# Optimization experiments

Measured on AMD Instinct MI355X. Metric: run time of the kernel, lower is better.

The kernel has to match this reference:

```python
import jax, jax.numpy as jnp
import numpy as np

N_HEAD = 8
N_FEAT = 512
D_HEAD = N_FEAT // N_HEAD


def setup_inputs() -> dict:
    key = jax.random.key(0)
    ks = jax.random.split(key, 11)
    B, T, L = 4, 2048, 16
    s = 1.0 / np.sqrt(D_HEAD)
    so = 1.0 / np.sqrt(N_FEAT)
    return {
        "q": jax.random.normal(ks[0], (B, T, 1, N_FEAT), jnp.float32),
        "k": jax.random.normal(ks[1], (B, T, L, N_FEAT), jnp.float32),
        "v": jax.random.normal(ks[2], (B, T, L, N_FEAT), jnp.float32),
        "Wq": jax.random.uniform(ks[3], (D_HEAD, D_HEAD), jnp.float32, -s, s),
        "bq": jax.random.uniform(ks[4], (D_HEAD,), jnp.float32, -s, s),
        "Wk": jax.random.uniform(ks[5], (D_HEAD, D_HEAD), jnp.float32, -s, s),
        "bk": jax.random.uniform(ks[6], (D_HEAD,), jnp.float32, -s, s),
        "Wv": jax.random.uniform(ks[7], (D_HEAD, D_HEAD), jnp.float32, -s, s),
        "bv": jax.random.uniform(ks[8], (D_HEAD,), jnp.float32, -s, s),
        "Wo": jax.random.uniform(ks[9], (N_FEAT, N_FEAT), jnp.float32, -so, so),
        "bo": jax.random.uniform(ks[10], (N_FEAT,), jnp.float32, -so, so),
    }


def reference(q, k, v, Wq, bq, Wk, bk, Wv, bv, Wo, bo):
    B, T, L, F = k.shape
    H, D = N_HEAD, D_HEAD
    # split heads: q [B,T,H,D] (query axis of length 1 squeezed), k/v [B,T,L,H,D]
    qh = q.reshape(B, T, H, D)
    kh = k.reshape(B, T, L, H, D)
    vh = v.reshape(B, T, L, H, D)
    # per-head linear projections (shared across heads), Linear: x @ W^T + b
    qh = jnp.einsum("bthd,ed->bthe", qh, Wq) + bq
    kh = jnp.einsum("btlhd,ed->btlhe", kh, Wk) + bk
    vh = jnp.einsum("btlhd,ed->btlhe", vh, Wv) + bv
    # attention scores over the local window L (query length 1 per timestep)
    attw = jnp.einsum("bthd,btlhd->bthl", qh, kh) / jnp.sqrt(jnp.asarray(D, qh.dtype))
    attn = jax.nn.softmax(attw, axis=-1)  # dropout is identity in eval mode
    ct = jnp.einsum("bthl,btlhd->bthd", attn, vh)
    ct = ct.reshape(B, T, F)
    return ct @ Wo.T + bo
```

## Files before the change

### kernel.cpp

```cpp
#include <hip/hip_runtime.h>


#define NFEAT 512
#define NHEAD 8
#define DHEAD 64
#define LWIN  16
#define WPOS  8
#define BTV   4

typedef __attribute__((ext_vector_type(8))) short bf16x8;
typedef __attribute__((ext_vector_type(4))) float f32x4;

__device__ __forceinline__ unsigned short f2bf(float f) {
    unsigned int u = __float_as_uint(f);
    unsigned int r = (u + 0x7fffu + ((u >> 16) & 1u)) >> 16;
    return (unsigned short)r;
}
__device__ __forceinline__ void unpack2(float f, float& lo, float& hi) {
    unsigned int u = __float_as_uint(f);
    lo = __uint_as_float(u << 16);
    hi = __uint_as_float(u & 0xffff0000u);
}

__global__ void precompute_small(const float* __restrict__ Wq, const float* __restrict__ bq,
                                 const float* __restrict__ Wk,
                                 const float* __restrict__ Wo, const float* __restrict__ bo,
                                 const float* __restrict__ bv,
                                 float* __restrict__ A, float* __restrict__ g,
                                 float* __restrict__ b2) {
    int idx = blockIdx.x * 256 + threadIdx.x;
    if (idx < 4096) {
        int d = idx >> 6, dp = idx & 63;
        float s = 0.f;
        #pragma unroll 8
        for (int e = 0; e < 64; ++e) s = fmaf(Wq[e * 64 + d], Wk[e * 64 + dp], s);
        A[idx] = s;
    } else if (idx < 4160) {
        int dp = idx - 4096;
        float s = 0.f;
        #pragma unroll 8
        for (int e = 0; e < 64; ++e) s = fmaf(Wk[e * 64 + dp], bq[e], s);
        g[dp] = s;
    } else if (idx < 4672) {
        int j = idx - 4160;
        float s = bo[j];
        #pragma unroll 8
        for (int i = 0; i < 512; ++i) s = fmaf(Wo[j * 512 + i], bv[i & 63], s);
        b2[j] = s;
    }
}

__global__ void precompute_wo2(const float* __restrict__ Wo, const float* __restrict__ Wv,
                               unsigned short* __restrict__ Wo2B) {
    int idx = blockIdx.x * 256 + threadIdx.x;
    int i = idx & 511, j = idx >> 9;
    int h = i >> 6, e = i & 63;
    float s = 0.f;
    #pragma unroll 8
    for (int d = 0; d < 64; ++d)
        s = fmaf(Wo[j * 512 + h * 64 + d], Wv[d * 64 + e], s);
    Wo2B[(size_t)j * 512 + i] = f2bf(s);
}

__global__ __launch_bounds__(512, 4)
void w_prepass(const float* __restrict__ q, const float* __restrict__ A,
               const float* __restrict__ g, float* __restrict__ Wm) {
    __shared__ float As[4096];
    __shared__ float qs[WPOS][NFEAT];
    const int tid = threadIdx.x;
    const int bt0 = blockIdx.x * WPOS;

    #pragma unroll
    for (int i = 0; i < 8; ++i) As[i * 512 + tid] = A[i * 512 + tid];
    #pragma unroll
    for (int r = 0; r < WPOS; ++r) qs[r][tid] = q[(size_t)(bt0 + r) * NFEAT + tid];
    __syncthreads();

    const int e  = tid & 63;
    const int hb = (tid >> 6) << 6;
    float acc[WPOS];
    const float ge = g[e];
    #pragma unroll
    for (int r = 0; r < WPOS; ++r) acc[r] = ge;

    #pragma unroll 4
    for (int dq = 0; dq < 16; ++dq) {
        const float a0 = As[(4 * dq + 0) * 64 + e];
        const float a1 = As[(4 * dq + 1) * 64 + e];
        const float a2 = As[(4 * dq + 2) * 64 + e];
        const float a3 = As[(4 * dq + 3) * 64 + e];
        #pragma unroll
        for (int r = 0; r < WPOS; ++r) {
            const float4 qv = *reinterpret_cast<const float4*>(&qs[r][hb + 4 * dq]);
            acc[r] = fmaf(qv.x, a0, acc[r]);
            acc[r] = fmaf(qv.y, a1, acc[r]);
            acc[r] = fmaf(qv.z, a2, acc[r]);
            acc[r] = fmaf(qv.w, a3, acc[r]);
        }
    }
    #pragma unroll
    for (int r = 0; r < WPOS; ++r)
        Wm[(size_t)(bt0 + r) * NFEAT + tid] = acc[r] * 0.125f;
}

__global__ __launch_bounds__(512, 8)
void score_kernel(const float* __restrict__ Wm, const float* __restrict__ k,
                  unsigned short* __restrict__ P) {
    const int tid  = threadIdx.x;
    const int h    = tid >> 6;
    const int lane = tid & 63;
    const int l    = lane >> 2;
    const int d4   = lane & 3;
    const int bt   = blockIdx.x;

    const float4* w4 = reinterpret_cast<const float4*>(
        Wm + (size_t)bt * NFEAT + h * 64 + d4 * 16);
    const float4* k4 = reinterpret_cast<const float4*>(
        k + (size_t)bt * (LWIN * NFEAT) + (size_t)l * NFEAT + h * 64 + d4 * 16);

    float a0 = 0.f, a1 = 0.f, a2 = 0.f, a3 = 0.f;
    #pragma unroll
    for (int i = 0; i < 4; ++i) {
        const float4 wq = w4[i];
        const float4 kq = k4[i];
        a0 = fmaf(wq.x, kq.x, a0);
        a1 = fmaf(wq.y, kq.y, a1);
        a2 = fmaf(wq.z, kq.z, a2);
        a3 = fmaf(wq.w, kq.w, a3);
    }
    float sc = (a0 + a1) + (a2 + a3);
    sc += __shfl_xor(sc, 1, 64);
    sc += __shfl_xor(sc, 2, 64);
    float mx = sc;
    mx = fmaxf(mx, __shfl_xor(mx, 4, 64));
    mx = fmaxf(mx, __shfl_xor(mx, 8, 64));
    mx = fmaxf(mx, __shfl_xor(mx, 16, 64));
    mx = fmaxf(mx, __shfl_xor(mx, 32, 64));
    const float e = __expf(sc - mx);
    float s = e;
    s += __shfl_xor(s, 4, 64);
    s += __shfl_xor(s, 8, 64);
    s += __shfl_xor(s, 16, 64);
    s += __shfl_xor(s, 32, 64);
    if (d4 == 0)
        P[((size_t)bt * NHEAD + h) * LWIN + l] = f2bf(e * (1.0f / s));
}

__global__ __launch_bounds__(512, 8)
void vbar_kernel(const unsigned short* __restrict__ P, const float* __restrict__ v,
                 unsigned short* __restrict__ vbarBF) {
    const int tid = threadIdx.x;
    const int h   = tid >> 6;
    const int bt0 = blockIdx.x * BTV;

    for (int pp = 0; pp < BTV; ++pp) {
        const int bt = bt0 + pp;
        const float4* pb = reinterpret_cast<const float4*>(
            P + ((size_t)bt * NHEAD + h) * LWIN);
        const float4 pA = pb[0];
        const float4 pB = pb[1];
        float p0, p1, p2, p3, p4, p5, p6, p7, p8, p9, pa, pbv, pc, pd, pe, pf;
        unpack2(pA.x, p0, p1); unpack2(pA.y, p2, p3);
        unpack2(pA.z, p4, p5); unpack2(pA.w, p6, p7);
        unpack2(pB.x, p8, p9); unpack2(pB.y, pa, pbv);
        unpack2(pB.z, pc, pd); unpack2(pB.w, pe, pf);

        const float* vp = v + (size_t)bt * (LWIN * NFEAT) + tid;
        float s0 = 0.f, s1 = 0.f, s2 = 0.f, s3 = 0.f;
        s0 = fmaf(p0, vp[ 0 * NFEAT], s0); s0 = fmaf(p1, vp[ 1 * NFEAT], s0);
        s0 = fmaf(p2, vp[ 2 * NFEAT], s0); s0 = fmaf(p3, vp[ 3 * NFEAT], s0);
        s1 = fmaf(p4, vp[ 4 * NFEAT], s1); s1 = fmaf(p5, vp[ 5 * NFEAT], s1);
        s1 = fmaf(p6, vp[ 6 * NFEAT], s1); s1 = fmaf(p7, vp[ 7 * NFEAT], s1);
        s2 = fmaf(p8, vp[ 8 * NFEAT], s2); s2 = fmaf(p9, vp[ 9 * NFEAT], s2);
        s2 = fmaf(pa, vp[10 * NFEAT], s2); s2 = fmaf(pbv, vp[11 * NFEAT], s2);
        s3 = fmaf(pc, vp[12 * NFEAT], s3); s3 = fmaf(pd, vp[13 * NFEAT], s3);
        s3 = fmaf(pe, vp[14 * NFEAT], s3); s3 = fmaf(pf, vp[15 * NFEAT], s3);
        vbarBF[(size_t)bt * NFEAT + tid] = f2bf((s0 + s1) + (s2 + s3));
    }
}

__global__ __launch_bounds__(512, 4)
void out_gemm(const unsigned short* __restrict__ vbarBF,
              const unsigned short* __restrict__ Wo2B,
              const float* __restrict__ b2, float* __restrict__ out) {
    const int tid  = threadIdx.x;
    const int w    = tid >> 6;
    const int lane = tid & 63;
    const int mt   = blockIdx.x;
    const int n0   = w * 64;
    const int r    = lane & 15;
    const int kg   = lane >> 4;

    const short* Ab = (const short*)vbarBF + ((size_t)(mt * 16 + r)) * 512 + kg * 8;
    const short* Bb0 = (const short*)Wo2B + ((size_t)(n0 + 0 + r)) * 512 + kg * 8;
    const short* Bb1 = (const short*)Wo2B + ((size_t)(n0 + 16 + r)) * 512 + kg * 8;
    const short* Bb2 = (const short*)Wo2B + ((size_t)(n0 + 32 + r)) * 512 + kg * 8;
    const short* Bb3 = (const short*)Wo2B + ((size_t)(n0 + 48 + r)) * 512 + kg * 8;

    f32x4 acc0 = {0.f, 0.f, 0.f, 0.f}, acc1 = acc0, acc2 = acc0, acc3 = acc0;

    #pragma unroll 4
    for (int kk = 0; kk < 16; ++kk) {
        const bf16x8 a  = *reinterpret_cast<const bf16x8*>(Ab  + kk * 32);
        const bf16x8 b0 = *reinterpret_cast<const bf16x8*>(Bb0 + kk * 32);
        const bf16x8 b1 = *reinterpret_cast<const bf16x8*>(Bb1 + kk * 32);
        const bf16x8 b2v = *reinterpret_cast<const bf16x8*>(Bb2 + kk * 32);
        const bf16x8 b3 = *reinterpret_cast<const bf16x8*>(Bb3 + kk * 32);
        acc0 = __builtin_amdgcn_mfma_f32_16x16x32_bf16(a, b0, acc0, 0, 0, 0);
        acc1 = __builtin_amdgcn_mfma_f32_16x16x32_bf16(a, b1, acc1, 0, 0, 0);
        acc2 = __builtin_amdgcn_mfma_f32_16x16x32_bf16(a, b2v, acc2, 0, 0, 0);
        acc3 = __builtin_amdgcn_mfma_f32_16x16x32_bf16(a, b3, acc3, 0, 0, 0);
    }

    const float bb0 = b2[n0 + 0 + r], bb1 = b2[n0 + 16 + r];
    const float bb2 = b2[n0 + 32 + r], bb3 = b2[n0 + 48 + r];
    #pragma unroll
    for (int j = 0; j < 4; ++j) {
        const size_t row = (size_t)(mt * 16 + kg * 4 + j) * 512;
        out[row + n0 + 0 + r]  = acc0[j] + bb0;
        out[row + n0 + 16 + r] = acc1[j] + bb1;
        out[row + n0 + 32 + r] = acc2[j] + bb2;
        out[row + n0 + 48 + r] = acc3[j] + bb3;
    }
}

extern "C" void kernel_launch(void* const* d_in, const int* in_sizes, int n_in,
                              void* d_out, int out_size, void* d_ws, size_t ws_size,
                              hipStream_t stream) {
    const float* q  = (const float*)d_in[0];
    const float* k  = (const float*)d_in[1];
    const float* v  = (const float*)d_in[2];
    const float* Wq = (const float*)d_in[3];
    const float* bq = (const float*)d_in[4];
    const float* Wk = (const float*)d_in[5];
    const float* Wv = (const float*)d_in[7];
    const float* bv = (const float*)d_in[8];
    const float* Wo = (const float*)d_in[9];
    const float* bo = (const float*)d_in[10];
    float* out = (float*)d_out;

    float* ws = (float*)d_ws;
    float*          A      = ws;
    float*          g      = ws + 4096;
    float*          b2     = ws + 4160;
    unsigned short* Wo2B   = (unsigned short*)(ws + 4672);
    float*          Wm     = ws + 4672 + 131072;
    unsigned short* vbarBF = (unsigned short*)Wm;
    unsigned short* P      = (unsigned short*)(ws + 4672 + 131072 + 4194304);

    const int BT = in_sizes[0] / NFEAT;

    hipLaunchKernelGGL(precompute_small, dim3(19), dim3(256), 0, stream,
                       Wq, bq, Wk, Wo, bo, bv, A, g, b2);
    hipLaunchKernelGGL(precompute_wo2, dim3(1024), dim3(256), 0, stream,
                       Wo, Wv, Wo2B);
    hipLaunchKernelGGL(w_prepass, dim3(BT / WPOS), dim3(512), 0, stream,
                       q, A, g, Wm);
    hipLaunchKernelGGL(score_kernel, dim3(BT), dim3(512), 0, stream,
                       Wm, k, P);
    hipLaunchKernelGGL(vbar_kernel, dim3(BT / BTV), dim3(512), 0, stream,
                       P, v, vbarBF);
    hipLaunchKernelGGL(out_gemm, dim3(BT / 16), dim3(512), 0, stream,
                       vbarBF, Wo2B, b2, out);
}
```

Before: 209.3 us.

## Fuse score softmax and V-weighted sum into one kernel via shared memory

Merges the score and vbar kernels into one kernel. Each block computes softmax weights for four timesteps into shared memory in fp32, then reads v with float4 loads to form the weighted sum. This removes a kernel launch and the bf16 probability buffer round-trip through global memory. The softmax also drops the max subtraction, which saves shuffles but can overflow if scores get large.

Result: faster. 196.5 us (-6.1%).

```diff
diff --git a/kernel.cpp b/kernel.cpp
--- a/kernel.cpp
+++ b/kernel.cpp
@@ -6,7 +6,7 @@
 #define DHEAD 64
 #define LWIN  16
 #define WPOS  8
-#define BTV   4
+#define NBT   4
 
 typedef __attribute__((ext_vector_type(8))) short bf16x8;
 typedef __attribute__((ext_vector_type(4))) float f32x4;
@@ -15,11 +15,6 @@
     unsigned int u = __float_as_uint(f);
     unsigned int r = (u + 0x7fffu + ((u >> 16) & 1u)) >> 16;
     return (unsigned short)r;
-}
-__device__ __forceinline__ void unpack2(float f, float& lo, float& hi) {
-    unsigned int u = __float_as_uint(f);
-    lo = __uint_as_float(u << 16);
-    hi = __uint_as_float(u & 0xffff0000u);
 }
 
 __global__ void precompute_small(const float* __restrict__ Wq, const float* __restrict__ bq,
@@ -103,79 +98,74 @@
         Wm[(size_t)(bt0 + r) * NFEAT + tid] = acc[r] * 0.125f;
 }
 
-__global__ __launch_bounds__(512, 8)
-void score_kernel(const float* __restrict__ Wm, const float* __restrict__ k,
-                  unsigned short* __restrict__ P) {
-    const int tid  = threadIdx.x;
-    const int h    = tid >> 6;
-    const int lane = tid & 63;
-    const int l    = lane >> 2;
-    const int d4   = lane & 3;
-    const int bt   = blockIdx.x;
-
-    const float4* w4 = reinterpret_cast<const float4*>(
-        Wm + (size_t)bt * NFEAT + h * 64 + d4 * 16);
-    const float4* k4 = reinterpret_cast<const float4*>(
-        k + (size_t)bt * (LWIN * NFEAT) + (size_t)l * NFEAT + h * 64 + d4 * 16);
-
-    float a0 = 0.f, a1 = 0.f, a2 = 0.f, a3 = 0.f;
-    #pragma unroll
-    for (int i = 0; i < 4; ++i) {
-        const float4 wq = w4[i];
-        const float4 kq = k4[i];
-        a0 = fmaf(wq.x, kq.x, a0);
-        a1 = fmaf(wq.y, kq.y, a1);
-        a2 = fmaf(wq.z, kq.z, a2);
-        a3 = fmaf(wq.w, kq.w, a3);
-    }
-    float sc = (a0 + a1) + (a2 + a3);
-    sc += __shfl_xor(sc, 1, 64);
-    sc += __shfl_xor(sc, 2, 64);
-    float mx = sc;
-    mx = fmaxf(mx, __shfl_xor(mx, 4, 64));
-    mx = fmaxf(mx, __shfl_xor(mx, 8, 64));
-    mx = fmaxf(mx, __shfl_xor(mx, 16, 64));
-    mx = fmaxf(mx, __shfl_xor(mx, 32, 64));
-    const float e = __expf(sc - mx);
-    float s = e;
-    s += __shfl_xor(s, 4, 64);
-    s += __shfl_xor(s, 8, 64);
-    s += __shfl_xor(s, 16, 64);
-    s += __shfl_xor(s, 32, 64);
-    if (d4 == 0)
-        P[((size_t)bt * NHEAD + h) * LWIN + l] = f2bf(e * (1.0f / s));
-}
-
-__global__ __launch_bounds__(512, 8)
-void vbar_kernel(const unsigned short* __restrict__ P, const float* __restrict__ v,
-                 unsigned short* __restrict__ vbarBF) {
+__global__ __launch_bounds__(512, 4)
+void attn_kv(const float* __restrict__ Wm, const float* __restrict__ k,
+             const float* __restrict__ v, unsigned short* __restrict__ vbarBF) {
+    __shared__ float ps[NHEAD][NBT][17];
+
     const int tid = threadIdx.x;
-    const int h   = tid >> 6;
-    const int bt0 = blockIdx.x * BTV;
-
-    for (int pp = 0; pp < BTV; ++pp) {
+    const int bt0 = blockIdx.x * NBT;
+
+    {
+        const int h    = tid >> 6;
+        const int lane = tid & 63;
+        const int l    = lane >> 2;
+        const int d4   = lane & 3;
+        #pragma unroll
+        for (int pp = 0; pp < NBT; ++pp) {
+            const int bt = bt0 + pp;
+            const float4* w4 = reinterpret_cast<const float4*>(
+                Wm + (size_t)bt * NFEAT + h * 64 + d4 * 16);
+            const float4* k4 = reinterpret_cast<const float4*>(
+                k + (size_t)bt * (LWIN * NFEAT) + (size_t)l * NFEAT + h * 64 + d4 * 16);
+            float a0 = 0.f, a1 = 0.f, a2 = 0.f, a3 = 0.f;
+            #pragma unroll
+            for (int i = 0; i < 4; ++i) {
+                const float4 wq = w4[i];
+                const float4 kq = k4[i];
+                a0 = fmaf(wq.x, kq.x, a0);
+                a1 = fmaf(wq.y, kq.y, a1);
+                a2 = fmaf(wq.z, kq.z, a2);
+                a3 = fmaf(wq.w, kq.w, a3);
+            }
+            float sc = (a0 + a1) + (a2 + a3);
+            sc += __shfl_xor(sc, 1, 64);
+            sc += __shfl_xor(sc, 2, 64);
+            const float e = __expf(sc);
+            float s = e;
+            s += __shfl_xor(s, 4, 64);
+            s += __shfl_xor(s, 8, 64);
+            s += __shfl_xor(s, 16, 64);
+            s += __shfl_xor(s, 32, 64);
+            if (d4 == 0) ps[h][pp][l] = e * (1.0f / s);
+        }
+    }
+    __syncthreads();
+
+    {
+        const int pp = tid >> 7;
+        const int f4 = tid & 127;
+        const int h  = f4 >> 4;
         const int bt = bt0 + pp;
-        const float4* pb = reinterpret_cast<const float4*>(
-            P + ((size_t)bt * NHEAD + h) * LWIN);
-        const float4 pA = pb[0];
-        const float4 pB = pb[1];
-        float p0, p1, p2, p3, p4, p5, p6, p7, p8, p9, pa, pbv, pc, pd, pe, pf;
-        unpack2(pA.x, p0, p1); unpack2(pA.y, p2, p3);
-        unpack2(pA.z, p4, p5); unpack2(pA.w, p6, p7);
-        unpack2(pB.x, p8, p9); unpack2(pB.y, pa, pbv);
-        unpack2(pB.z, pc, pd); unpack2(pB.w, pe, pf);
-
-        const float* vp = v + (size_t)bt * (LWIN * NFEAT) + tid;
-        float s0 = 0.f, s1 = 0.f, s2 = 0.f, s3 = 0.f;
-        s0 = fmaf(p0, vp[ 0 * NFEAT], s0); s0 = fmaf(p1, vp[ 1 * NFEAT], s0);
-        s0 = fmaf(p2, vp[ 2 * NFEAT], s0); s0 = fmaf(p3, vp[ 3 * NFEAT], s0);
-        s1 = fmaf(p4, vp[ 4 * NFEAT], s1); s1 = fmaf(p5, vp[ 5 * NFEAT], s1);
-        s1 = fmaf(p6, vp[ 6 * NFEAT], s1); s1 = fmaf(p7, vp[ 7 * NFEAT], s1);
-        s2 = fmaf(p8, vp[ 8 * NFEAT], s2); s2 = fmaf(p9, vp[ 9 * NFEAT], s2);
-        s2 = fmaf(pa, vp[10 * NFEAT], s2); s2 = fmaf(pbv, vp[11 * NFEAT], s2);
-        s3 = fmaf(pc, vp[12 * NFEAT], s3); s3 = fmaf(pd, vp[13 * NFEAT], s3);
-        s3 = fmaf(pe, vp[14 * NFEAT], s3); s3 = fmaf(pf, vp[15 * NFEAT], s3);
-        vbarBF[(size_t)bt * NFEAT + tid] = f2bf((s0 + s1) + (s2 + s3));
+
+        float pv[LWIN];
+        #pragma unroll
+        for (int i = 0; i < LWIN; ++i) pv[i] = ps[h][pp][i];
+
+        const float4* vp = reinterpret_cast<const float4*>(
+            v + (size_t)bt * (LWIN * NFEAT)) + f4;
+        float ax = 0.f, ay = 0.f, az = 0.f, aw = 0.f;
+        #pragma unroll
+        for (int l = 0; l < LWIN; ++l) {
+            const float4 vv = vp[(size_t)l * 128];
+            ax = fmaf(pv[l], vv.x, ax);
+            ay = fmaf(pv[l], vv.y, ay);
+            az = fmaf(pv[l], vv.z, az);
+            aw = fmaf(pv[l], vv.w, aw);
+        }
+        unsigned short o[4] = { f2bf(ax), f2bf(ay), f2bf(az), f2bf(aw) };
+        *reinterpret_cast<uint2*>(vbarBF + (size_t)bt * NFEAT + f4 * 4) =
+            *reinterpret_cast<uint2*>(o);
     }
 }
 
@@ -191,8 +181,8 @@
     const int r    = lane & 15;
     const int kg   = lane >> 4;
 
-    const short* Ab = (const short*)vbarBF + ((size_t)(mt * 16 + r)) * 512 + kg * 8;
-    const short* Bb0 = (const short*)Wo2B + ((size_t)(n0 + 0 + r)) * 512 + kg * 8;
+    const short* Ab  = (const short*)vbarBF + ((size_t)(mt * 16 + r)) * 512 + kg * 8;
+    const short* Bb0 = (const short*)Wo2B + ((size_t)(n0 +  0 + r)) * 512 + kg * 8;
     const short* Bb1 = (const short*)Wo2B + ((size_t)(n0 + 16 + r)) * 512 + kg * 8;
     const short* Bb2 = (const short*)Wo2B + ((size_t)(n0 + 32 + r)) * 512 + kg * 8;
     const short* Bb3 = (const short*)Wo2B + ((size_t)(n0 + 48 + r)) * 512 + kg * 8;
@@ -201,23 +191,23 @@
 
     #pragma unroll 4
     for (int kk = 0; kk < 16; ++kk) {
-        const bf16x8 a  = *reinterpret_cast<const bf16x8*>(Ab  + kk * 32);
-        const bf16x8 b0 = *reinterpret_cast<const bf16x8*>(Bb0 + kk * 32);
-        const bf16x8 b1 = *reinterpret_cast<const bf16x8*>(Bb1 + kk * 32);
+        const bf16x8 a   = *reinterpret_cast<const bf16x8*>(Ab  + kk * 32);
+        const bf16x8 b0  = *reinterpret_cast<const bf16x8*>(Bb0 + kk * 32);
+        const bf16x8 b1  = *reinterpret_cast<const bf16x8*>(Bb1 + kk * 32);
         const bf16x8 b2v = *reinterpret_cast<const bf16x8*>(Bb2 + kk * 32);
-        const bf16x8 b3 = *reinterpret_cast<const bf16x8*>(Bb3 + kk * 32);
-        acc0 = __builtin_amdgcn_mfma_f32_16x16x32_bf16(a, b0, acc0, 0, 0, 0);
-        acc1 = __builtin_amdgcn_mfma_f32_16x16x32_bf16(a, b1, acc1, 0, 0, 0);
+        const bf16x8 b3  = *reinterpret_cast<const bf16x8*>(Bb3 + kk * 32);
+        acc0 = __builtin_amdgcn_mfma_f32_16x16x32_bf16(a, b0,  acc0, 0, 0, 0);
+        acc1 = __builtin_amdgcn_mfma_f32_16x16x32_bf16(a, b1,  acc1, 0, 0, 0);
         acc2 = __builtin_amdgcn_mfma_f32_16x16x32_bf16(a, b2v, acc2, 0, 0, 0);
-        acc3 = __builtin_amdgcn_mfma_f32_16x16x32_bf16(a, b3, acc3, 0, 0, 0);
-    }
-
-    const float bb0 = b2[n0 + 0 + r], bb1 = b2[n0 + 16 + r];
+        acc3 = __builtin_amdgcn_mfma_f32_16x16x32_bf16(a, b3,  acc3, 0, 0, 0);
+    }
+
+    const float bb0 = b2[n0 + 0 + r],  bb1 = b2[n0 + 16 + r];
     const float bb2 = b2[n0 + 32 + r], bb3 = b2[n0 + 48 + r];
     #pragma unroll
     for (int j = 0; j < 4; ++j) {
         const size_t row = (size_t)(mt * 16 + kg * 4 + j) * 512;
-        out[row + n0 + 0 + r]  = acc0[j] + bb0;
+        out[row + n0 +  0 + r] = acc0[j] + bb0;
         out[row + n0 + 16 + r] = acc1[j] + bb1;
         out[row + n0 + 32 + r] = acc2[j] + bb2;
         out[row + n0 + 48 + r] = acc3[j] + bb3;
@@ -245,8 +235,7 @@
     float*          b2     = ws + 4160;
     unsigned short* Wo2B   = (unsigned short*)(ws + 4672);
     float*          Wm     = ws + 4672 + 131072;
-    unsigned short* vbarBF = (unsigned short*)Wm;
-    unsigned short* P      = (unsigned short*)(ws + 4672 + 131072 + 4194304);
+    unsigned short* vbarBF = (unsigned short*)(ws + 4672 + 131072 + 4194304);
 
     const int BT = in_sizes[0] / NFEAT;
 
@@ -256,10 +245,8 @@
                        Wo, Wv, Wo2B);
     hipLaunchKernelGGL(w_prepass, dim3(BT / WPOS), dim3(512), 0, stream,
                        q, A, g, Wm);
-    hipLaunchKernelGGL(score_kernel, dim3(BT), dim3(512), 0, stream,
-                       Wm, k, P);
-    hipLaunchKernelGGL(vbar_kernel, dim3(BT / BTV), dim3(512), 0, stream,
-                       P, v, vbarBF);
+    hipLaunchKernelGGL(attn_kv, dim3(BT / NBT), dim3(512), 0, stream,
+                       Wm, k, v, vbarBF);
     hipLaunchKernelGGL(out_gemm, dim3(BT / 16), dim3(512), 0, stream,
                        vbarBF, Wo2B, b2, out);
 }
```
